# Kernel tuning notes

Hardware: AMD Instinct MI355X
Metric: run time of the kernel (lower is better)

## Reference

```python
import jax, jax.numpy as jnp
import numpy as np

S, B, H, NH = 2048, 1, 1024, 16
HD = H // NH  # 64
NEG = float(np.finfo(np.float16).min)  # masked_fill value, matches torch.finfo(torch.float16).min


def setup_inputs() -> dict:
    key = jax.random.key(0)
    ks = jax.random.split(key, 9)
    w = lambda k: jax.random.normal(k, (H, H), jnp.float32) * 0.02
    b = lambda k: jax.random.normal(k, (H,), jnp.float32) * 0.01
    # causal (left-to-right) boolean mask, True = keep
    mask = jnp.tril(jnp.ones((S, S), dtype=bool))[None, None]  # [1,1,S,S]
    return {
        "hidden_states": jax.random.normal(ks[0], (S, B, H), jnp.float32),
        "Wq": w(ks[1]), "bq": b(ks[2]),
        "Wk": w(ks[3]), "bk": b(ks[4]),
        "Wv": w(ks[5]), "bv": b(ks[6]),
        "Wo": w(ks[7]), "bo": b(ks[8]),
        "attention_mask": mask,
    }


def reference(hidden_states, Wq, bq, Wk, bk, Wv, bv, Wo, bo, attention_mask):
    s, bsz, h = hidden_states.shape
    norm = float(np.sqrt(HD))
    # QKV projections (nn.Linear: x @ W.T + b), reshape to [S, B, NH, HD]
    q = (hidden_states @ Wq.T + bq).reshape(s, bsz, NH, HD) / norm
    k = (hidden_states @ Wk.T + bk).reshape(s, bsz, NH, HD)
    v = (hidden_states @ Wv.T + bv).reshape(s, bsz, NH, HD)
    # scores: [B, NH, S_q, S_kv] (baddbmm equivalent)
    scores = jnp.einsum('sbhd,tbhd->bhst', q, k)
    scores = jnp.where(attention_mask, scores, jnp.asarray(NEG, scores.dtype))
    # fp32 softmax, cast back to score dtype
    probs = jax.nn.softmax(scores.astype(jnp.float32), axis=-1).astype(scores.dtype)
    # context: [S, B, NH, HD] -> [S, B, H]
    ctx = jnp.einsum('bhst,tbhd->sbhd', probs, v).reshape(s, bsz, h)
    out = ctx @ Wo.T + bo
    return out
```

## Files before the change

### kernel.cpp

```cpp
#include <hip/hip_runtime.h>

typedef __attribute__((ext_vector_type(8))) short bf16x8;
typedef __attribute__((ext_vector_type(8))) unsigned short u16x8;
typedef __attribute__((ext_vector_type(4))) float f32x4;

#define GLDS16(SRC, DST) __builtin_amdgcn_global_load_lds( \
    (const __attribute__((address_space(1))) void*)(SRC),  \
    (__attribute__((address_space(3))) void*)(DST), 16, 0, 0)

__device__ __forceinline__ unsigned short f2bf(float f) {
  unsigned int u = __float_as_uint(f);
  u += 0x7FFFu + ((u >> 16) & 1u);
  return (unsigned short)(u >> 16);
}
__device__ __forceinline__ float bf2f(unsigned short u) {
  return __uint_as_float((unsigned int)u << 16);
}

__global__ void cvt_all(const float* __restrict__ hid,
                        const float* __restrict__ Wq, const float* __restrict__ Wk,
                        const float* __restrict__ Wv, const float* __restrict__ Wo,
                        const float* __restrict__ bq, const float* __restrict__ bk,
                        const float* __restrict__ bv,
                        unsigned short* __restrict__ hb, unsigned short* __restrict__ Wcat,
                        unsigned short* __restrict__ Wob, float* __restrict__ bcat) {
  const int H4 = 2048 * 1024 / 4, W4 = 1024 * 1024 / 4;
  int i = blockIdx.x * 256 + threadIdx.x;
  const float* src; unsigned short* dst; float scale = 1.0f; int j;
  if (i < H4)                { src = hid; dst = hb;                 j = i; }
  else if (i < H4 + W4)      { src = Wq;  dst = Wcat;               j = i - H4; scale = 0.125f; }
  else if (i < H4 + 2 * W4)  { src = Wk;  dst = Wcat + 1024 * 1024; j = i - H4 - W4; }
  else if (i < H4 + 3 * W4)  { src = Wv;  dst = Wcat + 2048 * 1024; j = i - H4 - 2 * W4; }
  else if (i < H4 + 4 * W4)  { src = Wo;  dst = Wob;                j = i - H4 - 3 * W4; }
  else {
    j = i - H4 - 4 * W4;
    int e = j * 4;
    const float* b = (e < 1024) ? bq : (e < 2048 ? bk + (-1024) : bv + (-2048));
    float4 v = *(const float4*)(b + e);
    if (e < 1024) { v.x *= 0.125f; v.y *= 0.125f; v.z *= 0.125f; v.w *= 0.125f; }
    ((float4*)bcat)[j] = v;
    return;
  }
  float4 v = ((const float4*)src)[j];
  ushort4 o;
  o.x = f2bf(v.x * scale); o.y = f2bf(v.y * scale);
  o.z = f2bf(v.z * scale); o.w = f2bf(v.w * scale);
  ((ushort4*)dst)[j] = o;
}

template <int BM, int BN, typename OutT>
__global__ __launch_bounds__(256) void gemm_bt(
    const unsigned short* __restrict__ A, const unsigned short* __restrict__ B,
    const float* __restrict__ bias, OutT* __restrict__ C,
    int M, int N, int K, int lda, int ldb, int ldc)
{
  constexpr int MREP = BM / 32, NREP = BN / 32;
  __shared__ __align__(16) unsigned short As[2][BM * 32];
  __shared__ __align__(16) unsigned short Bs[2][BN * 32];
  const int t = threadIdx.x;
  const int lane = t & 63;
  const int w = t >> 6;
  const int wm = w >> 1, wn = w & 1;
  const int lr = lane & 15, lk = lane >> 4;
  const int tm = blockIdx.y * BM, tn = blockIdx.x * BN;

  f32x4 acc[MREP][NREP];
#pragma unroll
  for (int m = 0; m < MREP; ++m)
#pragma unroll
    for (int n = 0; n < NREP; ++n) acc[m][n] = (f32x4){0.f, 0.f, 0.f, 0.f};

  const int ra0 = t >> 2;
  const int ka0 = (t & 3) << 3;
  const int ra1 = 64 + (t >> 2);
  const int lds0 = (t & 192) * 8;
  const int lds1 = (256 + (t & 192)) * 8;

  const int NT = K >> 5;
  GLDS16(A + (size_t)(tm + ra0) * lda + ka0, &As[0][lds0]);
  if constexpr (BM == 128) GLDS16(A + (size_t)(tm + ra1) * lda + ka0, &As[0][lds1]);
  GLDS16(B + (size_t)(tn + ra0) * ldb + ka0, &Bs[0][lds0]);
  if constexpr (BN == 128) GLDS16(B + (size_t)(tn + ra1) * ldb + ka0, &Bs[0][lds1]);
  __syncthreads();

  for (int kt = 0; kt < NT; ++kt) {
    const int cur = kt & 1, nxt = cur ^ 1;
    if (kt + 1 < NT) {
      const int k0 = (kt + 1) << 5;
      GLDS16(A + (size_t)(tm + ra0) * lda + k0 + ka0, &As[nxt][lds0]);
      if constexpr (BM == 128) GLDS16(A + (size_t)(tm + ra1) * lda + k0 + ka0, &As[nxt][lds1]);
      GLDS16(B + (size_t)(tn + ra0) * ldb + k0 + ka0, &Bs[nxt][lds0]);
      if constexpr (BN == 128) GLDS16(B + (size_t)(tn + ra1) * ldb + k0 + ka0, &Bs[nxt][lds1]);
    }
    bf16x8 af[MREP], bfv[NREP];
#pragma unroll
    for (int m = 0; m < MREP; ++m)
      af[m] = *(const bf16x8*)&As[cur][(wm * (BM / 2) + m * 16 + lr) * 32 + lk * 8];
#pragma unroll
    for (int n = 0; n < NREP; ++n)
      bfv[n] = *(const bf16x8*)&Bs[cur][(wn * (BN / 2) + n * 16 + lr) * 32 + lk * 8];
#pragma unroll
    for (int m = 0; m < MREP; ++m)
#pragma unroll
      for (int n = 0; n < NREP; ++n)
        acc[m][n] = __builtin_amdgcn_mfma_f32_16x16x32_bf16(af[m], bfv[n], acc[m][n], 0, 0, 0);
    __syncthreads();
  }

#pragma unroll
  for (int m = 0; m < MREP; ++m) {
    const int row0 = tm + wm * (BM / 2) + m * 16 + lk * 4;
#pragma unroll
    for (int n = 0; n < NREP; ++n) {
      const int col = tn + wn * (BN / 2) + n * 16 + lr;
      const float bb = bias ? bias[col] : 0.f;
#pragma unroll
      for (int r = 0; r < 4; ++r) {
        float v = acc[m][n][r] + bb;
        if constexpr (sizeof(OutT) == 2) {
          ((unsigned short*)C)[(size_t)(row0 + r) * ldc + col] = f2bf(v);
        } else {
          ((float*)C)[(size_t)(row0 + r) * ldc + col] = v;
        }
      }
    }
  }
}

__device__ __forceinline__ int slot_off(int qt) {
  int g = qt >> 2;
  return (g == 1) ? (qt - 4) * 2 : (g == 2) ? 8 + (qt - 8) * 3 : 20 + (qt - 12) * 4;
}

__global__ __launch_bounds__(512, 4) void attn_fwd(const unsigned short* __restrict__ QKV,
                                                   unsigned short* __restrict__ ctx,
                                                   unsigned short* __restrict__ Opart,
                                                   float* __restrict__ mlbuf)
{
  __shared__ __align__(16) unsigned short Ks[2][64 * 64];
  __shared__ __align__(16) unsigned short Vt[2][64 * 64];
  __shared__ __align__(16) unsigned int   Pl[8][16 * 36];

  const int t = threadIdx.x;
  const int lane = t & 63, w = t >> 6;
  const int lr = lane & 15, lk = lane >> 4;
  const int h = blockIdx.y;
  const int p = 39 - (int)blockIdx.x;
  int qt, c;
  if (p < 4)       { qt = p; c = 0; }
  else if (p < 12) { qt = 4 + ((p - 4) >> 1); c = (p - 4) & 1; }
  else if (p < 24) { int r = p - 12; qt = 8 + r / 3; c = r - (r / 3) * 3; }
  else             { int r = p - 24; qt = 12 + (r >> 2); c = r & 3; }
  const int nc = (qt >> 2) + 1;
  const int q0 = qt * 128;
  const int qd = 2 * qt + 1;
  const size_t ldq = 3072;

  const unsigned short* qbase = QKV + (size_t)(q0 + w * 16 + lr) * ldq + h * 64;
  const bf16x8 qf0 = *(const bf16x8*)(qbase + lk * 8);
  const bf16x8 qf1 = *(const bf16x8*)(qbase + 32 + lk * 8);
  const int qglob = q0 + w * 16 + lr;

  f32x4 acc[4];
#pragma unroll
  for (int d = 0; d < 4; ++d) acc[d] = (f32x4){0.f, 0.f, 0.f, 0.f};
  float mrun = -__builtin_inff(), lrun = 0.f;

  const int srow = t >> 3;
  const int sslot = t & 7;
  const int scol = (sslot ^ (srow & 7)) << 3;
  const int ldsb = (t & 448) * 8;

  const unsigned short* kbase = QKV + 1024 + h * 64;
  const unsigned short* vbase = QKV + 2048 + h * 64;

  const int kt0 = c * 8;
  const int kt1 = (qd < kt0 + 7) ? qd : kt0 + 7;

  {
    const int kv0 = kt0 * 64;
    GLDS16(kbase + (size_t)(kv0 + srow) * ldq + scol, &Ks[0][ldsb]);
    const bf16x8 v0 = *(const bf16x8*)(vbase + (size_t)(kv0 + srow) * ldq + (sslot << 3));
    const int d0 = sslot << 3;
#pragma unroll
    for (int j = 0; j < 8; ++j) {
      const int d = d0 + j;
      const int key = (d ^ (d >> 3)) & 7;
      Vt[0][d * 64 + (((srow >> 3) ^ key) << 3) + (srow & 7)] = (unsigned short)v0[j];
    }
  }
  __syncthreads();

  int cur = 0;
  for (int kt = kt0; kt <= kt1; ++kt) {
    const bool more = kt < kt1;
    bf16x8 vnxt;
    if (more) {
      const int kvn = (kt + 1) * 64;
      GLDS16(kbase + (size_t)(kvn + srow) * ldq + scol, &Ks[cur ^ 1][ldsb]);
      vnxt = *(const bf16x8*)(vbase + (size_t)(kvn + srow) * ldq + (sslot << 3));
    }

    const int kv0 = kt * 64;
    f32x4 sacc[4];
    __builtin_amdgcn_s_setprio(1);
#pragma unroll
    for (int sub = 0; sub < 4; ++sub) {
      const int krow = sub * 16 + lr;
      const int sw = krow & 7;
      const bf16x8 kf0 = *(const bf16x8*)&Ks[cur][krow * 64 + ((lk ^ sw) << 3)];
      const bf16x8 kf1 = *(const bf16x8*)&Ks[cur][krow * 64 + (((4 + lk) ^ sw) << 3)];
      f32x4 s = (f32x4){0.f, 0.f, 0.f, 0.f};
      s = __builtin_amdgcn_mfma_f32_16x16x32_bf16(kf0, qf0, s, 0, 0, 0);
      s = __builtin_amdgcn_mfma_f32_16x16x32_bf16(kf1, qf1, s, 0, 0, 0);
      sacc[sub] = s;
    }
    __builtin_amdgcn_s_setprio(0);

    if (kt + 1 >= qd) {
#pragma unroll
      for (int sub = 0; sub < 4; ++sub) {
#pragma unroll
        for (int r = 0; r < 4; ++r)
          if (kv0 + sub * 16 + lk * 4 + r > qglob) sacc[sub][r] = -__builtin_inff();
      }
    }

    float pm = -__builtin_inff();
#pragma unroll
    for (int sub = 0; sub < 4; ++sub)
#pragma unroll
      for (int r = 0; r < 4; ++r) pm = fmaxf(pm, sacc[sub][r]);
    pm = fmaxf(pm, __shfl_xor(pm, 16, 64));
    pm = fmaxf(pm, __shfl_xor(pm, 32, 64));
    const float mnew = fmaxf(mrun, pm);
    const float sc = __expf(mrun - mnew);
    lrun *= sc;
#pragma unroll
    for (int d = 0; d < 4; ++d) acc[d] *= sc;
    float pp[4][4]; float rs = 0.f;
#pragma unroll
    for (int sub = 0; sub < 4; ++sub)
#pragma unroll
      for (int r = 0; r < 4; ++r) { pp[sub][r] = __expf(sacc[sub][r] - mnew); rs += pp[sub][r]; }
    rs += __shfl_xor(rs, 16, 64);
    rs += __shfl_xor(rs, 32, 64);
    lrun += rs;
    mrun = mnew;

    unsigned int* prow = &Pl[w][lr * 36];
#pragma unroll
    for (int sub = 0; sub < 4; ++sub) {
#pragma unroll
      for (int j = 0; j < 2; ++j) {
        unsigned int pk;
        asm("v_cvt_pk_bf16_f32 %0, %1, %2" : "=v"(pk) : "v"(pp[sub][2 * j]), "v"(pp[sub][2 * j + 1]));
        prow[sub * 8 + lk * 2 + j] = pk;
      }
    }
    asm volatile("s_waitcnt lgkmcnt(0)" ::: "memory");
    __builtin_amdgcn_sched_barrier(0);

    const bf16x8 pb0 = *(const bf16x8*)&Pl[w][lr * 36 + lk * 4];
    const bf16x8 pb1 = *(const bf16x8*)&Pl[w][lr * 36 + 16 + lk * 4];
    __builtin_amdgcn_s_setprio(1);
#pragma unroll
    for (int dsub = 0; dsub < 4; ++dsub) {
      const int dd = dsub * 16 + lr;
      const int key = (dd ^ (dd >> 3)) & 7;
      const bf16x8 bv0 = *(const bf16x8*)&Vt[cur][dd * 64 + ((lk ^ key) << 3)];
      const bf16x8 bv1 = *(const bf16x8*)&Vt[cur][dd * 64 + (((4 + lk) ^ key) << 3)];
      acc[dsub] = __builtin_amdgcn_mfma_f32_16x16x32_bf16(bv0, pb0, acc[dsub], 0, 0, 0);
      acc[dsub] = __builtin_amdgcn_mfma_f32_16x16x32_bf16(bv1, pb1, acc[dsub], 0, 0, 0);
    }
    __builtin_amdgcn_s_setprio(0);

    if (more) {
      const int d0 = sslot << 3;
      const int nxt = cur ^ 1;
#pragma unroll
      for (int j = 0; j < 8; ++j) {
        const int d = d0 + j;
        const int key = (d ^ (d >> 3)) & 7;
        Vt[nxt][d * 64 + (((srow >> 3) ^ key) << 3) + (srow & 7)] = (unsigned short)vnxt[j];
      }
      __syncthreads();
      cur = nxt;
    }
  }

  if (nc == 1) {
    const float inv = 1.0f / lrun;
#pragma unroll
    for (int dsub = 0; dsub < 4; ++dsub) {
      ushort4 o;
      o.x = f2bf(acc[dsub][0] * inv);
      o.y = f2bf(acc[dsub][1] * inv);
      o.z = f2bf(acc[dsub][2] * inv);
      o.w = f2bf(acc[dsub][3] * inv);
      *(ushort4*)&ctx[(size_t)qglob * 1024 + h * 64 + dsub * 16 + lk * 4] = o;
    }
  } else {
    const int slot = h * 36 + slot_off(qt) + c;
    unsigned short* Op = Opart + (size_t)slot * 8192;
    const int ql = w * 16 + lr;
#pragma unroll
    for (int dsub = 0; dsub < 4; ++dsub) {
      ushort4 o;
      o.x = f2bf(acc[dsub][0]);
      o.y = f2bf(acc[dsub][1]);
      o.z = f2bf(acc[dsub][2]);
      o.w = f2bf(acc[dsub][3]);
      *(ushort4*)&Op[ql * 64 + dsub * 16 + lk * 4] = o;
    }
    if (lk == 0)
      *(float2*)&mlbuf[(slot * 128 + ql) * 2] = make_float2(mrun, lrun);
  }
}

template <int NC>
__device__ __forceinline__ void combine_body(const unsigned short* __restrict__ Opart,
                                             const float* __restrict__ mlbuf,
                                             unsigned short* __restrict__ ctx,
                                             int qt, int quarter, int h, int t) {
  const int q = quarter * 32 + (t >> 3);
  const int d0 = (t & 7) * 8;
  const int slot0 = h * 36 + slot_off(qt);
  float m[NC], l[NC];
#pragma unroll
  for (int c = 0; c < NC; ++c) {
    const float2 ml = *(const float2*)&mlbuf[((slot0 + c) * 128 + q) * 2];
    m[c] = ml.x; l[c] = ml.y;
  }
  float M = m[0];
#pragma unroll
  for (int c = 1; c < NC; ++c) M = fmaxf(M, m[c]);
  float wgt[NC], L = 0.f;
#pragma unroll
  for (int c = 0; c < NC; ++c) { wgt[c] = __expf(m[c] - M); L += wgt[c] * l[c]; }
  u16x8 v[NC];
#pragma unroll
  for (int c = 0; c < NC; ++c)
    v[c] = *(const u16x8*)&Opart[(size_t)(slot0 + c) * 8192 + q * 64 + d0];
  const float inv = 1.0f / L;
  u16x8 r;
#pragma unroll
  for (int j = 0; j < 8; ++j) {
    float o = 0.f;
#pragma unroll
    for (int c = 0; c < NC; ++c) o += wgt[c] * bf2f(v[c][j]);
    r[j] = f2bf(o * inv);
  }
  *(u16x8*)&ctx[(size_t)(qt * 128 + q) * 1024 + h * 64 + d0] = r;
}

__global__ __launch_bounds__(256) void attn_combine(const unsigned short* __restrict__ Opart,
                                                    const float* __restrict__ mlbuf,
                                                    unsigned short* __restrict__ ctx) {
  const int t = threadIdx.x;
  const int h = blockIdx.y;
  const int idx = blockIdx.x;
  const int g = idx >> 4;
  const int i = idx & 15;
  const int qt = 4 + g * 4 + (i >> 2);
  const int quarter = i & 3;
  if (g == 0)      combine_body<2>(Opart, mlbuf, ctx, qt, quarter, h, t);
  else if (g == 1) combine_body<3>(Opart, mlbuf, ctx, qt, quarter, h, t);
  else             combine_body<4>(Opart, mlbuf, ctx, qt, quarter, h, t);
}

extern "C" void kernel_launch(void* const* d_in, const int* in_sizes, int n_in,
                              void* d_out, int out_size, void* d_ws, size_t ws_size,
                              hipStream_t stream) {
  const float* hid = (const float*)d_in[0];
  const float* Wq  = (const float*)d_in[1];
  const float* bq  = (const float*)d_in[2];
  const float* Wk  = (const float*)d_in[3];
  const float* bk  = (const float*)d_in[4];
  const float* Wv  = (const float*)d_in[5];
  const float* bv  = (const float*)d_in[6];
  const float* Wo  = (const float*)d_in[7];
  const float* bo  = (const float*)d_in[8];
  float* out = (float*)d_out;

  char* ws = (char*)d_ws;
  unsigned short* hb   = (unsigned short*)(ws);
  unsigned short* Wcat = (unsigned short*)(ws + (4u  << 20));
  unsigned short* Wob  = (unsigned short*)(ws + (10u << 20));
  float*          bcat = (float*)         (ws + (12u << 20));
  unsigned short* QKV  = (unsigned short*)(ws + (13u << 20));
  unsigned short* ctx  = (unsigned short*)(ws + (25u << 20));
  unsigned short* Opart = (unsigned short*)(ws);
  float*          mlbuf = (float*)(ws + 9437184);

  cvt_all<<<6147, 256, 0, stream>>>(hid, Wq, Wk, Wv, Wo, bq, bk, bv,
                                    hb, Wcat, Wob, bcat);

  gemm_bt<64, 128, unsigned short><<<dim3(24, 32), 256, 0, stream>>>(
      hb, Wcat, bcat, QKV, 2048, 3072, 1024, 1024, 1024, 3072);

  attn_fwd<<<dim3(40, 16), 512, 0, stream>>>(QKV, ctx, Opart, mlbuf);

  attn_combine<<<dim3(48, 16), 256, 0, stream>>>(Opart, mlbuf, ctx);

  gemm_bt<64, 64, float><<<dim3(16, 32), 256, 0, stream>>>(
      ctx, Wob, bo, out, 2048, 1024, 1024, 1024, 1024, 1024);
}
```

Measured before the change: 86.24 us.

## Fuse split-KV combine into attention via atomic last-block reduction and lazy rescale

Removes the separate attn_combine launch. Each split-KV block now writes its partial output, then bumps a per-(head, q-tile) atomic counter, and the last block to arrive merges all partials into ctx. The counters are zeroed inside the existing conversion kernel. Separately, the online softmax now skips the running-max rescale unless some row's new max exceeds the old one by more than 8, which saves exps and multiplies at the cost of a small precision margin. Together these trade one kernel launch and some softmax work for a threadfence/atomic tail in the attention kernel.

```diff
diff --git a/kernel.cpp b/kernel.cpp
--- a/kernel.cpp
+++ b/kernel.cpp
@@ -23,7 +23,8 @@
                         const float* __restrict__ bq, const float* __restrict__ bk,
                         const float* __restrict__ bv,
                         unsigned short* __restrict__ hb, unsigned short* __restrict__ Wcat,
-                        unsigned short* __restrict__ Wob, float* __restrict__ bcat) {
+                        unsigned short* __restrict__ Wob, float* __restrict__ bcat,
+                        int* __restrict__ cnt) {
   const int H4 = 2048 * 1024 / 4, W4 = 1024 * 1024 / 4;
   int i = blockIdx.x * 256 + threadIdx.x;
   const float* src; unsigned short* dst; float scale = 1.0f; int j;
@@ -34,11 +35,16 @@
   else if (i < H4 + 4 * W4)  { src = Wo;  dst = Wob;                j = i - H4 - 3 * W4; }
   else {
     j = i - H4 - 4 * W4;
-    int e = j * 4;
-    const float* b = (e < 1024) ? bq : (e < 2048 ? bk + (-1024) : bv + (-2048));
-    float4 v = *(const float4*)(b + e);
-    if (e < 1024) { v.x *= 0.125f; v.y *= 0.125f; v.z *= 0.125f; v.w *= 0.125f; }
-    ((float4*)bcat)[j] = v;
+    if (j < 768) {
+      int e = j * 4;
+      const float* b = (e < 1024) ? bq : (e < 2048 ? bk + (-1024) : bv + (-2048));
+      float4 v = *(const float4*)(b + e);
+      if (e < 1024) { v.x *= 0.125f; v.y *= 0.125f; v.z *= 0.125f; v.w *= 0.125f; }
+      ((float4*)bcat)[j] = v;
+    } else {
+      int k = j - 768;
+      if (k < 256) cnt[k] = 0;
+    }
     return;
   }
   float4 v = ((const float4*)src)[j];
@@ -135,11 +141,13 @@
 __global__ __launch_bounds__(512, 4) void attn_fwd(const unsigned short* __restrict__ QKV,
                                                    unsigned short* __restrict__ ctx,
                                                    unsigned short* __restrict__ Opart,
-                                                   float* __restrict__ mlbuf)
+                                                   float* __restrict__ mlbuf,
+                                                   int* __restrict__ cnt)
 {
   __shared__ __align__(16) unsigned short Ks[2][64 * 64];
   __shared__ __align__(16) unsigned short Vt[2][64 * 64];
   __shared__ __align__(16) unsigned int   Pl[8][16 * 36];
+  __shared__ int lastflag;
 
   const int t = threadIdx.x;
   const int lane = t & 63, w = t >> 6;
@@ -233,20 +241,22 @@
       for (int r = 0; r < 4; ++r) pm = fmaxf(pm, sacc[sub][r]);
     pm = fmaxf(pm, __shfl_xor(pm, 16, 64));
     pm = fmaxf(pm, __shfl_xor(pm, 32, 64));
-    const float mnew = fmaxf(mrun, pm);
-    const float sc = __expf(mrun - mnew);
-    lrun *= sc;
-#pragma unroll
-    for (int d = 0; d < 4; ++d) acc[d] *= sc;
+    if (!__all(pm <= mrun + 8.0f)) {
+      const float mnew = fmaxf(mrun, pm);
+      const float sc = __expf(mrun - mnew);
+      lrun *= sc;
+#pragma unroll
+      for (int d = 0; d < 4; ++d) acc[d] *= sc;
+      mrun = mnew;
+    }
     float pp[4][4]; float rs = 0.f;
 #pragma unroll
     for (int sub = 0; sub < 4; ++sub)
 #pragma unroll
-      for (int r = 0; r < 4; ++r) { pp[sub][r] = __expf(sacc[sub][r] - mnew); rs += pp[sub][r]; }
+      for (int r = 0; r < 4; ++r) { pp[sub][r] = __expf(sacc[sub][r] - mrun); rs += pp[sub][r]; }
     rs += __shfl_xor(rs, 16, 64);
     rs += __shfl_xor(rs, 32, 64);
     lrun += rs;
-    mrun = mnew;
 
     unsigned int* prow = &Pl[w][lr * 36];
 #pragma unroll
@@ -300,73 +310,66 @@
       o.w = f2bf(acc[dsub][3] * inv);
       *(ushort4*)&ctx[(size_t)qglob * 1024 + h * 64 + dsub * 16 + lk * 4] = o;
     }
-  } else {
-    const int slot = h * 36 + slot_off(qt) + c;
-    unsigned short* Op = Opart + (size_t)slot * 8192;
-    const int ql = w * 16 + lr;
-#pragma unroll
-    for (int dsub = 0; dsub < 4; ++dsub) {
-      ushort4 o;
-      o.x = f2bf(acc[dsub][0]);
-      o.y = f2bf(acc[dsub][1]);
-      o.z = f2bf(acc[dsub][2]);
-      o.w = f2bf(acc[dsub][3]);
-      *(ushort4*)&Op[ql * 64 + dsub * 16 + lk * 4] = o;
-    }
-    if (lk == 0)
-      *(float2*)&mlbuf[(slot * 128 + ql) * 2] = make_float2(mrun, lrun);
-  }
-}
-
-template <int NC>
-__device__ __forceinline__ void combine_body(const unsigned short* __restrict__ Opart,
-                                             const float* __restrict__ mlbuf,
-                                             unsigned short* __restrict__ ctx,
-                                             int qt, int quarter, int h, int t) {
-  const int q = quarter * 32 + (t >> 3);
-  const int d0 = (t & 7) * 8;
+    return;
+  }
+
+  const int slot = h * 36 + slot_off(qt) + c;
+  unsigned short* Op = Opart + (size_t)slot * 8192;
+  const int ql = w * 16 + lr;
+#pragma unroll
+  for (int dsub = 0; dsub < 4; ++dsub) {
+    ushort4 o;
+    o.x = f2bf(acc[dsub][0]);
+    o.y = f2bf(acc[dsub][1]);
+    o.z = f2bf(acc[dsub][2]);
+    o.w = f2bf(acc[dsub][3]);
+    *(ushort4*)&Op[ql * 64 + dsub * 16 + lk * 4] = o;
+  }
+  if (lk == 0)
+    *(float2*)&mlbuf[(slot * 128 + ql) * 2] = make_float2(mrun, lrun);
+
+  __syncthreads();
+  if (t == 0) {
+    __threadfence();
+    int old = atomicAdd(&cnt[h * 16 + qt], 1);
+    lastflag = (old == nc - 1) ? 1 : 0;
+  }
+  __syncthreads();
+  if (!lastflag) return;
+  __threadfence();
+
   const int slot0 = h * 36 + slot_off(qt);
-  float m[NC], l[NC];
-#pragma unroll
-  for (int c = 0; c < NC; ++c) {
-    const float2 ml = *(const float2*)&mlbuf[((slot0 + c) * 128 + q) * 2];
-    m[c] = ml.x; l[c] = ml.y;
-  }
-  float M = m[0];
-#pragma unroll
-  for (int c = 1; c < NC; ++c) M = fmaxf(M, m[c]);
-  float wgt[NC], L = 0.f;
-#pragma unroll
-  for (int c = 0; c < NC; ++c) { wgt[c] = __expf(m[c] - M); L += wgt[c] * l[c]; }
-  u16x8 v[NC];
-#pragma unroll
-  for (int c = 0; c < NC; ++c)
-    v[c] = *(const u16x8*)&Opart[(size_t)(slot0 + c) * 8192 + q * 64 + d0];
+  const int q = t >> 2;
+  const int d0 = (t & 3) << 4;
+  float mm[4], ll[4];
+  float M = -__builtin_inff();
+#pragma unroll
+  for (int cc = 0; cc < 4; ++cc)
+    if (cc < nc) {
+      const float2 ml = *(const float2*)&mlbuf[((slot0 + cc) * 128 + q) * 2];
+      mm[cc] = ml.x; ll[cc] = ml.y;
+      M = fmaxf(M, mm[cc]);
+    }
+  float wgt[4], L = 0.f;
+#pragma unroll
+  for (int cc = 0; cc < 4; ++cc)
+    if (cc < nc) { wgt[cc] = __expf(mm[cc] - M); L += wgt[cc] * ll[cc]; }
   const float inv = 1.0f / L;
-  u16x8 r;
-#pragma unroll
-  for (int j = 0; j < 8; ++j) {
-    float o = 0.f;
-#pragma unroll
-    for (int c = 0; c < NC; ++c) o += wgt[c] * bf2f(v[c][j]);
-    r[j] = f2bf(o * inv);
-  }
-  *(u16x8*)&ctx[(size_t)(qt * 128 + q) * 1024 + h * 64 + d0] = r;
-}
-
-__global__ __launch_bounds__(256) void attn_combine(const unsigned short* __restrict__ Opart,
-                                                    const float* __restrict__ mlbuf,
-                                                    unsigned short* __restrict__ ctx) {
-  const int t = threadIdx.x;
-  const int h = blockIdx.y;
-  const int idx = blockIdx.x;
-  const int g = idx >> 4;
-  const int i = idx & 15;
-  const int qt = 4 + g * 4 + (i >> 2);
-  const int quarter = i & 3;
-  if (g == 0)      combine_body<2>(Opart, mlbuf, ctx, qt, quarter, h, t);
-  else if (g == 1) combine_body<3>(Opart, mlbuf, ctx, qt, quarter, h, t);
-  else             combine_body<4>(Opart, mlbuf, ctx, qt, quarter, h, t);
+#pragma unroll
+  for (int half = 0; half < 2; ++half) {
+    float o[8] = {0.f, 0.f, 0.f, 0.f, 0.f, 0.f, 0.f, 0.f};
+#pragma unroll
+    for (int cc = 0; cc < 4; ++cc)
+      if (cc < nc) {
+        const u16x8 v = *(const u16x8*)&Opart[(size_t)(slot0 + cc) * 8192 + q * 64 + d0 + half * 8];
+#pragma unroll
+        for (int j = 0; j < 8; ++j) o[j] += wgt[cc] * bf2f(v[j]);
+      }
+    u16x8 r;
+#pragma unroll
+    for (int j = 0; j < 8; ++j) r[j] = f2bf(o[j] * inv);
+    *(u16x8*)&ctx[(size_t)(qt * 128 + q) * 1024 + h * 64 + d0 + half * 8] = r;
+  }
 }
 
 extern "C" void kernel_launch(void* const* d_in, const int* in_sizes, int n_in,
@@ -390,18 +393,17 @@
   float*          bcat = (float*)         (ws + (12u << 20));
   unsigned short* QKV  = (unsigned short*)(ws + (13u << 20));
   unsigned short* ctx  = (unsigned short*)(ws + (25u << 20));
+  int*            cnt  = (int*)           (ws + (29u << 20));
   unsigned short* Opart = (unsigned short*)(ws);
   float*          mlbuf = (float*)(ws + 9437184);
 
-  cvt_all<<<6147, 256, 0, stream>>>(hid, Wq, Wk, Wv, Wo, bq, bk, bv,
-                                    hb, Wcat, Wob, bcat);
+  cvt_all<<<6148, 256, 0, stream>>>(hid, Wq, Wk, Wv, Wo, bq, bk, bv,
+                                    hb, Wcat, Wob, bcat, cnt);
 
   gemm_bt<64, 128, unsigned short><<<dim3(24, 32), 256, 0, stream>>>(
       hb, Wcat, bcat, QKV, 2048, 3072, 1024, 1024, 1024, 3072);
 
-  attn_fwd<<<dim3(40, 16), 512, 0, stream>>>(QKV, ctx, Opart, mlbuf);
-
-  attn_combine<<<dim3(48, 16), 256, 0, stream>>>(Opart, mlbuf, ctx);
+  attn_fwd<<<dim3(40, 16), 512, 0, stream>>>(QKV, ctx, Opart, mlbuf, cnt);
 
   gemm_bt<64, 64, float><<<dim3(16, 32), 256, 0, stream>>>(
       ctx, Wob, bo, out, 2048, 1024, 1024, 1024, 1024, 1024);
```

Result: slower. 173.3 us (+101.0%).
